# Kernel optimization log

Measured on AMD Instinct MI355X. Metric: run time of the kernel, lower is better.

## Reference

```python
import jax, jax.numpy as jnp
import numpy as np

N, LN, S, T = 50000, 64, 8, 4
E = 800000
MU = 0.9


def setup_inputs() -> dict:
    key = jax.random.key(0)
    ks = jax.random.split(key, 10)
    X_Node = jax.random.randint(ks[0], (E,), 0, N, dtype=jnp.int64) if jax.config.jax_enable_x64 else jax.random.randint(ks[0], (E,), 0, N).astype(jnp.int32)
    X_Neis = jax.random.randint(ks[1], (E,), 0, N).astype(X_Node.dtype)
    dg_list = jax.random.randint(ks[2], (E,), 1, 64).astype(jnp.float32)
    sc = 0.05
    W_emb = jax.random.normal(ks[3], (N, LN), jnp.float32) * sc
    Wxi = jax.random.normal(ks[4], (2 * LN, S * S), jnp.float32) * sc
    bxi = jnp.zeros((S * S,), jnp.float32)
    Wrou = jax.random.normal(ks[5], (LN, S), jnp.float32) * sc
    brou = jnp.zeros((S,), jnp.float32)
    Wout = jax.random.normal(ks[6], (LN + S, 3), jnp.float32) * sc
    bout = jnp.zeros((3,), jnp.float32)
    return {"X_Node": X_Node, "X_Neis": X_Neis, "dg_list": dg_list,
            "W_emb": W_emb, "Wxi": Wxi, "bxi": bxi,
            "Wrou": Wrou, "brou": brou, "Wout": Wout, "bout": bout}


def reference(X_Node, X_Neis, dg_list, W_emb, Wxi, bxi, Wrou, brou, Wout, bout):
    # Edge-wise feature gather: X = [emb[src] || emb[dst]]  -> [E, 2*LN]
    node_e = W_emb[X_Node]
    neis_e = W_emb[X_Neis]
    X = jnp.concatenate([node_e, neis_e], axis=1)
    # Hw precompute (loop-invariant): A [E,S,S], b [E,S]
    A = jnp.tanh(X @ Wxi + bxi).reshape(-1, S, S) * (MU / S) / dg_list[:, None, None]
    b = jnp.tanh(node_e @ Wrou + brou)

    states = jnp.zeros((N, S), dtype=W_emb.dtype)

    def step(states, _):
        H = states[X_Node]                      # gather [E, S]
        H = jnp.einsum('eij,ej->ei', A, H) + b  # per-edge small matvec
        # AggrSum's one-hot [V,E] matmul == scatter-add by X_Node
        new_states = jax.ops.segment_sum(H, X_Node, num_segments=N)
        return new_states, None

    states, _ = jax.lax.scan(step, states, None, length=T)
    logits = jnp.concatenate([W_emb, states], axis=1) @ Wout + bout
    return jax.nn.softmax(logits, axis=1)
```

## Files before the change

### kernel.cpp

```cpp
#include <hip/hip_runtime.h>
#include <hip/hip_fp16.h>
#include <math.h>

#define N_NODES 50000
#define LNDIM   64
#define E_EDGES 800000
#define MU_OVER_S 0.1125f
#define HPAD 16
#define NRANGE 8
#define RANGE_SZ ((N_NODES + NRANGE - 1) / NRANGE)
#define MAXDEG 48
#define BCAP 110000
#define PRE_TPB 256
#define PRE_TILES ((N_NODES + PRE_TPB - 1) / PRE_TPB)
#define LDS_STRIDE 257
#define BK_EPT 16
#define BK_EPB (256 * BK_EPT)
#define BK_NB ((E_EDGES + BK_EPB - 1) / BK_EPB)
#define LOG2E 1.4426950408889634f

typedef _Float16 h2 __attribute__((ext_vector_type(2)));
typedef __fp16   fp16x2 __attribute__((ext_vector_type(2)));

__device__ __forceinline__ h2 bits_h2(unsigned u) {
    union { unsigned x; h2 h; } c; c.x = u; return c.h;
}
__device__ __forceinline__ unsigned h2_bits(h2 h) {
    union { h2 h; unsigned x; } c; c.h = h; return c.x;
}
__device__ __forceinline__ unsigned h2_bits(fp16x2 h) {
    union { fp16x2 h; unsigned x; } c; c.h = h; return c.x;
}

__global__ __launch_bounds__(256) void zero_kernel(int4* __restrict__ p, int n4)
{
    int i = blockIdx.x * 256 + threadIdx.x;
    if (i < n4) p[i] = make_int4(0, 0, 0, 0);
}

__global__ __launch_bounds__(256, 4) void fused_kernel(
    const float* __restrict__ W_emb, const float* __restrict__ Wxi,
    const float* __restrict__ bxi,   const float* __restrict__ Wrou,
    const float* __restrict__ brou,
    const int* __restrict__ X_Node, const int* __restrict__ X_Neis,
    const float* __restrict__ dg_list,
    unsigned short* __restrict__ T1, unsigned short* __restrict__ U,
    float* __restrict__ Bv, int* __restrict__ bkt_cursor,
    uint2* __restrict__ pairs)
{
    __shared__ float ldsT[32 * LDS_STRIDE];
    __shared__ int scnt[4][NRANGE];
    __shared__ int wpref[4][NRANGE];
    __shared__ int gbase[NRANGE];

    int tid = threadIdx.x;

    if (blockIdx.x < BK_NB) {
        int lane = tid & 63;
        int wid  = tid >> 6;
        int wavebase = blockIdx.x * BK_EPB + wid * (BK_EPT * 64);

        unsigned nd[BK_EPT], py[BK_EPT];
        int wcnt[NRANGE];
        #pragma unroll
        for (int r = 0; r < NRANGE; ++r) wcnt[r] = 0;

        #pragma unroll
        for (int i = 0; i < BK_EPT; ++i) {
            int e  = wavebase + i * 64 + lane;
            bool ok = e < E_EDGES;
            int ec = ok ? e : (E_EDGES - 1);
            int node = X_Node[ec];
            unsigned nei = (unsigned)X_Neis[ec];
            float sc = MU_OVER_S / dg_list[ec];
            __half_raw hr = __half_raw(__float2half(sc));
            py[i] = nei | ((unsigned)hr.x << 16);
            int r = ok ? (node / RANGE_SZ) : NRANGE;
            nd[i] = (unsigned)node | ((unsigned)r << 24);
            #pragma unroll
            for (int rr = 0; rr < NRANGE; ++rr)
                wcnt[rr] += __popcll(__ballot(r == rr));
        }

        if (lane < NRANGE) scnt[wid][lane] = wcnt[lane];
        __syncthreads();
        if (tid < NRANGE) {
            int c0 = scnt[0][tid], c1 = scnt[1][tid], c2 = scnt[2][tid], c3 = scnt[3][tid];
            wpref[0][tid] = 0;
            wpref[1][tid] = c0;
            wpref[2][tid] = c0 + c1;
            wpref[3][tid] = c0 + c1 + c2;
            gbase[tid] = atomicAdd(&bkt_cursor[tid * HPAD], c0 + c1 + c2 + c3);
        }
        __syncthreads();

        int wb[NRANGE];
        #pragma unroll
        for (int r = 0; r < NRANGE; ++r) wb[r] = gbase[r] + wpref[wid][r];

        #pragma unroll
        for (int i = 0; i < BK_EPT; ++i) {
            int r = nd[i] >> 24;
            #pragma unroll
            for (int rr = 0; rr < NRANGE; ++rr) {
                unsigned long long m = __ballot(r == rr);
                if (r == rr) {
                    int rank = __popcll(m & ((1ULL << lane) - 1ULL));
                    int pos  = wb[rr] + rank;
                    if (pos < BCAP)
                        pairs[(size_t)rr * BCAP + pos] =
                            make_uint2(nd[i] & 0xFFFFFFu, py[i]);
                }
                wb[rr] += __popcll(m);
            }
        }
        return;
    }

    int pb   = blockIdx.x - BK_NB;
    int pass = pb / PRE_TILES;
    int tile = pb % PRE_TILES;
    int base = tile * PRE_TPB;
    int v    = base + tid;

    if (pass == 4) {
        float acc[8];
        #pragma unroll
        for (int j = 0; j < 8; ++j) acc[j] = brou[j];
        for (int kc = 0; kc < 2; ++kc) {
            __syncthreads();
            #pragma unroll
            for (int c = 0; c < 8; ++c) {
                int idx  = c * PRE_TPB + tid;
                int node = idx >> 3, part = idx & 7;
                int nn   = min(base + node, N_NODES - 1);
                float4 q = *(const float4*)(W_emb + (size_t)nn * 64 + kc * 32 + part * 4);
                ldsT[(part*4+0)*LDS_STRIDE + node] = q.x;
                ldsT[(part*4+1)*LDS_STRIDE + node] = q.y;
                ldsT[(part*4+2)*LDS_STRIDE + node] = q.z;
                ldsT[(part*4+3)*LDS_STRIDE + node] = q.w;
            }
            __syncthreads();
            for (int kk = 0; kk < 32; ++kk) {
                float ek = ldsT[kk * LDS_STRIDE + tid];
                const float* wr = Wrou + (kc*32 + kk) * 8;
                #pragma unroll
                for (int j = 0; j < 8; ++j) acc[j] = fmaf(ek, wr[j], acc[j]);
            }
        }
        if (v < N_NODES) {
            float4* dst = (float4*)(Bv + (size_t)v * 8);
            dst[0] = make_float4(tanhf(acc[0]), tanhf(acc[1]), tanhf(acc[2]), tanhf(acc[3]));
            dst[1] = make_float4(tanhf(acc[4]), tanhf(acc[5]), tanhf(acc[6]), tanhf(acc[7]));
        }
        return;
    }

    int is_u  = pass >> 1;
    int jbase = (pass & 1) * 32;
    const float* W = Wxi + (is_u ? 64 * 64 : 0) + jbase;
    float acc[32];
    if (is_u) {
        #pragma unroll
        for (int j = 0; j < 32; ++j) acc[j] = 0.f;
    } else {
        #pragma unroll
        for (int j = 0; j < 32; ++j) acc[j] = bxi[jbase + j];
    }
    for (int kc = 0; kc < 2; ++kc) {
        __syncthreads();
        #pragma unroll
        for (int c = 0; c < 8; ++c) {
            int idx  = c * PRE_TPB + tid;
            int node = idx >> 3, part = idx & 7;
            int nn   = min(base + node, N_NODES - 1);
            float4 q = *(const float4*)(W_emb + (size_t)nn * 64 + kc * 32 + part * 4);
            ldsT[(part*4+0)*LDS_STRIDE + node] = q.x;
            ldsT[(part*4+1)*LDS_STRIDE + node] = q.y;
            ldsT[(part*4+2)*LDS_STRIDE + node] = q.z;
            ldsT[(part*4+3)*LDS_STRIDE + node] = q.w;
        }
        __syncthreads();
        for (int kk = 0; kk < 32; ++kk) {
            float ek = ldsT[kk * LDS_STRIDE + tid];
            const float* wr = W + (kc*32 + kk) * 64;
            #pragma unroll
            for (int j = 0; j < 32; ++j) acc[j] = fmaf(ek, wr[j], acc[j]);
        }
    }
    if (v >= N_NODES) return;
    unsigned short* outp = is_u ? U : T1;
    uint4* dst = (uint4*)(outp + (size_t)v * 64 + jbase);
    #pragma unroll
    for (int t = 0; t < 4; ++t) {
        uint4 q;
        q.x = h2_bits(__builtin_amdgcn_cvt_pkrtz(acc[8*t+0], acc[8*t+1]));
        q.y = h2_bits(__builtin_amdgcn_cvt_pkrtz(acc[8*t+2], acc[8*t+3]));
        q.z = h2_bits(__builtin_amdgcn_cvt_pkrtz(acc[8*t+4], acc[8*t+5]));
        q.w = h2_bits(__builtin_amdgcn_cvt_pkrtz(acc[8*t+6], acc[8*t+7]));
        dst[t] = q;
    }
}

__global__ __launch_bounds__(256) void scatter2_kernel(
    const uint2* __restrict__ pairs, const int* __restrict__ bkt_cursor,
    int* __restrict__ cnt_arr, unsigned* __restrict__ pk_s)
{
    int r = blockIdx.x & (NRANGE - 1);
    int i = (blockIdx.x >> 3) * 256 + threadIdx.x;
    if (i >= bkt_cursor[r * HPAD]) return;
    uint2 p = pairs[(size_t)r * BCAP + i];
    int pos = atomicAdd(&cnt_arr[(size_t)p.x * HPAD], 1);
    if (pos < MAXDEG) pk_s[(size_t)p.x * MAXDEG + pos] = p.y;
}

__global__ __launch_bounds__(256, 4) void main_kernel(
    const float* __restrict__ W_emb, const float* __restrict__ Wout,
    const float* __restrict__ bout,
    const unsigned short* __restrict__ T1, const unsigned short* __restrict__ U,
    const float* __restrict__ Bv, const int* __restrict__ cnt_arr,
    const unsigned* __restrict__ pk_s, float* __restrict__ out)
{
    int lane = threadIdx.x & 63;
    int wid  = threadIdx.x >> 6;
    int v    = blockIdx.x * 4 + wid;
    if (v >= N_NODES) return;

    int cntv = min(cnt_arr[(size_t)v * HPAD], MAXDEG);
    unsigned pkl = (lane < MAXDEG) ? pk_s[(size_t)v * MAXDEG + lane] : 0u;
    unsigned pk  = (lane < cntv) ? pkl : 0u;
    unsigned tu  = (unsigned)T1[(size_t)v * 64 + lane];
    h2 t2 = bits_h2(tu | (tu << 16));

    const h2 c1 = { (_Float16)0.13333334f,  (_Float16)0.13333334f };
    const h2 c0 = { (_Float16)-0.33333334f, (_Float16)-0.33333334f };

    float m0 = 0.f, m1 = 0.f;

    for (int k0 = 0; k0 < cntv; k0 += 16) {
        unsigned q[16], uu[16];
        #pragma unroll
        for (int x = 0; x < 16; ++x) {
            q[x]  = (unsigned)__builtin_amdgcn_readlane((int)pk, k0 + x);
            uu[x] = (unsigned)U[(size_t)(q[x] & 0xFFFFu) * 64 + lane];
        }
        __builtin_amdgcn_sched_barrier(0);
        #pragma unroll
        for (int p = 0; p < 8; ++p) {
            unsigned sc2 = (q[2*p] >> 16) | (q[2*p+1] & 0xFFFF0000u);
            h2 x   = bits_h2(uu[2*p] | (uu[2*p+1] << 16)) + t2;
            h2 x2  = x * x;
            h2 a   = x2 * c1 + c0;
            h2 th  = (x * x2) * a + x;
            if (p & 1) m1 = __builtin_amdgcn_fdot2(th, bits_h2(sc2), m1, false);
            else       m0 = __builtin_amdgcn_fdot2(th, bits_h2(sc2), m0, false);
        }
    }
    float macc = m0 + m1;

    int   j   = lane & 7;
    int   i   = lane >> 3;
    float cnt = (float)cntv;
    float cj  = cnt * Bv[v * 8 + j];
    float ci  = __shfl(cj, i);
    float sj  = cj;

    #pragma unroll
    for (int step = 0; step < 3; ++step) {
        float p = macc * sj;
        p += __shfl_xor(p, 1);
        p += __shfl_xor(p, 2);
        p += __shfl_xor(p, 4);
        float snew = p + ci;
        sj = __shfl(snew, j * 8);
    }

    float emb = W_emb[(size_t)v * 64 + lane];
    float p0 = emb * Wout[lane * 3 + 0];
    float p1 = emb * Wout[lane * 3 + 1];
    float p2 = emb * Wout[lane * 3 + 2];
    if (lane < 8) {
        p0 = fmaf(sj, Wout[(64 + lane) * 3 + 0], p0);
        p1 = fmaf(sj, Wout[(64 + lane) * 3 + 1], p1);
        p2 = fmaf(sj, Wout[(64 + lane) * 3 + 2], p2);
    }
    #pragma unroll
    for (int m = 1; m < 64; m <<= 1) {
        p0 += __shfl_xor(p0, m);
        p1 += __shfl_xor(p1, m);
        p2 += __shfl_xor(p2, m);
    }
    float L0 = p0 + bout[0], L1 = p1 + bout[1], L2 = p2 + bout[2];
    float mx = fmaxf(L0, fmaxf(L1, L2));
    float e0 = __builtin_amdgcn_exp2f((L0 - mx) * LOG2E);
    float e1 = __builtin_amdgcn_exp2f((L1 - mx) * LOG2E);
    float e2 = __builtin_amdgcn_exp2f((L2 - mx) * LOG2E);
    float inv = __builtin_amdgcn_rcpf(e0 + e1 + e2);
    float rr = (lane == 0) ? e0 : (lane == 1 ? e1 : e2);
    if (lane < 3) out[v * 3 + lane] = rr * inv;
}

extern "C" void kernel_launch(void* const* d_in, const int* in_sizes, int n_in,
                              void* d_out, int out_size, void* d_ws, size_t ws_size,
                              hipStream_t stream)
{
    const int*   X_Node = (const int*)  d_in[0];
    const int*   X_Neis = (const int*)  d_in[1];
    const float* dg     = (const float*)d_in[2];
    const float* W_emb  = (const float*)d_in[3];
    const float* Wxi    = (const float*)d_in[4];
    const float* bxi    = (const float*)d_in[5];
    const float* Wrou   = (const float*)d_in[6];
    const float* brou   = (const float*)d_in[7];
    const float* Wout   = (const float*)d_in[8];
    const float* bout   = (const float*)d_in[9];
    float*       out    = (float*)d_out;

    char*  ws  = (char*)d_ws;
    size_t off = 0;
    auto alloc = [&](size_t bytes) -> void* {
        void* p = ws + off;
        off += (bytes + 255) & ~(size_t)255;
        return p;
    };
    unsigned short* T1       = (unsigned short*)alloc((size_t)N_NODES * 64 * 2);
    unsigned short* U        = (unsigned short*)alloc((size_t)N_NODES * 64 * 2);
    float*          Bv       = (float*)alloc((size_t)N_NODES * 8 * 4);
    int*            cnt_arr  = (int*)  alloc((size_t)N_NODES * HPAD * 4);
    int*            bkt_cur  = (int*)  alloc((size_t)NRANGE * HPAD * 4);
    uint2*          pairs    = (uint2*)alloc((size_t)NRANGE * BCAP * 8);
    unsigned*       pk_s     = (unsigned*)alloc(((size_t)N_NODES * MAXDEG + 64) * 4);

    const int NZ4 = (N_NODES * HPAD + NRANGE * HPAD) / 4;

    zero_kernel<<<(NZ4 + 255) / 256, 256, 0, stream>>>((int4*)cnt_arr, NZ4);
    fused_kernel<<<BK_NB + PRE_TILES * 5, 256, 0, stream>>>(
        W_emb, Wxi, bxi, Wrou, brou, X_Node, X_Neis, dg,
        T1, U, Bv, bkt_cur, pairs);
    scatter2_kernel<<<((BCAP + 255) / 256) * NRANGE, 256, 0, stream>>>(
        pairs, bkt_cur, cnt_arr, pk_s);
    main_kernel<<<(N_NODES + 3) / 4, 256, 0, stream>>>(
        W_emb, Wout, bout, T1, U, Bv, cnt_arr, pk_s, out);
}
```

Baseline: 103.0 us.

## Compute node-level Wxi projections with bf16 MFMA instead of scalar FMAs

Replaces the scalar LDS-transposed fp32 GEMM that built the per-node T1/U projection tables with a wave-level bf16 MFMA (16x16x32) path. Wxi is pre-packed into the MFMA B-operand layout by a prep kernel, which also absorbs the old zeroing kernel. The Wrou/Bv projection becomes its own simple per-thread pass that reads directly from global memory. The aim is to cut the ALU-bound precompute cost and one launch. The trade-off is reduced precision from bf16 inputs and scattered 2-byte output stores.

```diff
diff --git a/kernel.cpp b/kernel.cpp
--- a/kernel.cpp
+++ b/kernel.cpp
@@ -11,44 +11,55 @@
 #define RANGE_SZ ((N_NODES + NRANGE - 1) / NRANGE)
 #define MAXDEG 48
 #define BCAP 110000
-#define PRE_TPB 256
-#define PRE_TILES ((N_NODES + PRE_TPB - 1) / PRE_TPB)
-#define LDS_STRIDE 257
 #define BK_EPT 16
 #define BK_EPB (256 * BK_EPT)
 #define BK_NB ((E_EDGES + BK_EPB - 1) / BK_EPB)
+#define GEMM_NB ((N_NODES + 63) / 64)
+#define BV_TILES ((N_NODES + 255) / 256)
 #define LOG2E 1.4426950408889634f
 
 typedef _Float16 h2 __attribute__((ext_vector_type(2)));
-typedef __fp16   fp16x2 __attribute__((ext_vector_type(2)));
-
+typedef short    bf16x8 __attribute__((ext_vector_type(8)));
+typedef float    f32x4  __attribute__((ext_vector_type(4)));
+
+__device__ __forceinline__ unsigned short f2bf(float f) {
+    unsigned int u = __float_as_uint(f);
+    u = (u + 0x7FFFu + ((u >> 16) & 1u)) >> 16;
+    return (unsigned short)u;
+}
 __device__ __forceinline__ h2 bits_h2(unsigned u) {
     union { unsigned x; h2 h; } c; c.x = u; return c.h;
 }
-__device__ __forceinline__ unsigned h2_bits(h2 h) {
-    union { h2 h; unsigned x; } c; c.h = h; return c.x;
-}
-__device__ __forceinline__ unsigned h2_bits(fp16x2 h) {
-    union { fp16x2 h; unsigned x; } c; c.h = h; return c.x;
-}
-
-__global__ __launch_bounds__(256) void zero_kernel(int4* __restrict__ p, int n4)
-{
-    int i = blockIdx.x * 256 + threadIdx.x;
-    if (i < n4) p[i] = make_int4(0, 0, 0, 0);
+
+__global__ __launch_bounds__(256) void prep_kernel(
+    const float* __restrict__ Wxi, unsigned short* __restrict__ Bpk,
+    int4* __restrict__ zp, int nz4)
+{
+    int gid = blockIdx.x * 256 + threadIdx.x;
+    if (gid < 8192) {
+        int jt = gid >> 10;
+        int rem = gid & 1023;
+        int h = rem >> 9;
+        int rem2 = rem & 511;
+        int l = rem2 >> 3, i = rem2 & 7;
+        int k   = h * 32 + (l >> 4) * 8 + i;
+        int row = (jt >= 4 ? 64 : 0) + k;
+        int col = (jt & 3) * 16 + (l & 15);
+        Bpk[gid] = f2bf(Wxi[row * 64 + col]);
+    }
+    if (gid < nz4) zp[gid] = make_int4(0, 0, 0, 0);
 }
 
 __global__ __launch_bounds__(256, 4) void fused_kernel(
-    const float* __restrict__ W_emb, const float* __restrict__ Wxi,
-    const float* __restrict__ bxi,   const float* __restrict__ Wrou,
-    const float* __restrict__ brou,
+    const float* __restrict__ W_emb, const float* __restrict__ bxi,
+    const float* __restrict__ Wrou,  const float* __restrict__ brou,
     const int* __restrict__ X_Node, const int* __restrict__ X_Neis,
     const float* __restrict__ dg_list,
+    const unsigned short* __restrict__ Bpk,
     unsigned short* __restrict__ T1, unsigned short* __restrict__ U,
-    float* __restrict__ Bv, int* __restrict__ bkt_cursor,
-    uint2* __restrict__ pairs)
-{
-    __shared__ float ldsT[32 * LDS_STRIDE];
+    float* __restrict__ Bv,
+    int* __restrict__ bkt_cursor, uint2* __restrict__ pairs)
+{
     __shared__ int scnt[4][NRANGE];
     __shared__ int wpref[4][NRANGE];
     __shared__ int gbase[NRANGE];
@@ -117,89 +128,82 @@
         return;
     }
 
-    int pb   = blockIdx.x - BK_NB;
-    int pass = pb / PRE_TILES;
-    int tile = pb % PRE_TILES;
-    int base = tile * PRE_TPB;
-    int v    = base + tid;
-
-    if (pass == 4) {
-        float acc[8];
-        #pragma unroll
-        for (int j = 0; j < 8; ++j) acc[j] = brou[j];
-        for (int kc = 0; kc < 2; ++kc) {
-            __syncthreads();
-            #pragma unroll
-            for (int c = 0; c < 8; ++c) {
-                int idx  = c * PRE_TPB + tid;
-                int node = idx >> 3, part = idx & 7;
-                int nn   = min(base + node, N_NODES - 1);
-                float4 q = *(const float4*)(W_emb + (size_t)nn * 64 + kc * 32 + part * 4);
-                ldsT[(part*4+0)*LDS_STRIDE + node] = q.x;
-                ldsT[(part*4+1)*LDS_STRIDE + node] = q.y;
-                ldsT[(part*4+2)*LDS_STRIDE + node] = q.z;
-                ldsT[(part*4+3)*LDS_STRIDE + node] = q.w;
+    if (blockIdx.x < BK_NB + GEMM_NB) {
+        int gb   = blockIdx.x - BK_NB;
+        int lane = tid & 63;
+        int wid  = tid >> 6;
+        int nodebase = gb * 64 + wid * 16;
+        if (nodebase >= N_NODES) return;
+
+        int r0 = lane & 15;
+        int g  = lane >> 4;
+
+        bf16x8 a[2];
+        int arow = min(nodebase + r0, N_NODES - 1);
+        const float* ap = W_emb + (size_t)arow * 64 + g * 8;
+        #pragma unroll
+        for (int h = 0; h < 2; ++h) {
+            float4 q0 = *(const float4*)(ap + h * 32);
+            float4 q1 = *(const float4*)(ap + h * 32 + 4);
+            bf16x8 t;
+            t[0] = (short)f2bf(q0.x); t[1] = (short)f2bf(q0.y);
+            t[2] = (short)f2bf(q0.z); t[3] = (short)f2bf(q0.w);
+            t[4] = (short)f2bf(q1.x); t[5] = (short)f2bf(q1.y);
+            t[6] = (short)f2bf(q1.z); t[7] = (short)f2bf(q1.w);
+            a[h] = t;
+        }
+
+        #pragma unroll
+        for (int jt = 0; jt < 8; ++jt) {
+            float binit = (jt < 4) ? bxi[(jt & 3) * 16 + r0] : 0.f;
+            f32x4 acc;
+            acc[0] = binit; acc[1] = binit; acc[2] = binit; acc[3] = binit;
+            #pragma unroll
+            for (int h = 0; h < 2; ++h) {
+                bf16x8 b = *(const bf16x8*)(Bpk + ((size_t)(jt * 2 + h) * 64 + lane) * 8);
+                acc = __builtin_amdgcn_mfma_f32_16x16x32_bf16(a[h], b, acc, 0, 0, 0);
             }
-            __syncthreads();
-            for (int kk = 0; kk < 32; ++kk) {
-                float ek = ldsT[kk * LDS_STRIDE + tid];
-                const float* wr = Wrou + (kc*32 + kk) * 8;
-                #pragma unroll
-                for (int j = 0; j < 8; ++j) acc[j] = fmaf(ek, wr[j], acc[j]);
+            unsigned short* outp = (jt < 4) ? T1 : U;
+            int jcol = (jt & 3) * 16 + r0;
+            #pragma unroll
+            for (int r = 0; r < 4; ++r) {
+                int node = nodebase + g * 4 + r;
+                if (node < N_NODES) {
+                    union { _Float16 h; unsigned short u; } cv;
+                    cv.h = (_Float16)acc[r];
+                    outp[(size_t)node * 64 + jcol] = cv.u;
+                }
             }
         }
-        if (v < N_NODES) {
-            float4* dst = (float4*)(Bv + (size_t)v * 8);
-            dst[0] = make_float4(tanhf(acc[0]), tanhf(acc[1]), tanhf(acc[2]), tanhf(acc[3]));
-            dst[1] = make_float4(tanhf(acc[4]), tanhf(acc[5]), tanhf(acc[6]), tanhf(acc[7]));
-        }
         return;
     }
 
-    int is_u  = pass >> 1;
-    int jbase = (pass & 1) * 32;
-    const float* W = Wxi + (is_u ? 64 * 64 : 0) + jbase;
-    float acc[32];
-    if (is_u) {
-        #pragma unroll
-        for (int j = 0; j < 32; ++j) acc[j] = 0.f;
-    } else {
-        #pragma unroll
-        for (int j = 0; j < 32; ++j) acc[j] = bxi[jbase + j];
-    }
-    for (int kc = 0; kc < 2; ++kc) {
-        __syncthreads();
-        #pragma unroll
-        for (int c = 0; c < 8; ++c) {
-            int idx  = c * PRE_TPB + tid;
-            int node = idx >> 3, part = idx & 7;
-            int nn   = min(base + node, N_NODES - 1);
-            float4 q = *(const float4*)(W_emb + (size_t)nn * 64 + kc * 32 + part * 4);
-            ldsT[(part*4+0)*LDS_STRIDE + node] = q.x;
-            ldsT[(part*4+1)*LDS_STRIDE + node] = q.y;
-            ldsT[(part*4+2)*LDS_STRIDE + node] = q.z;
-            ldsT[(part*4+3)*LDS_STRIDE + node] = q.w;
-        }
-        __syncthreads();
-        for (int kk = 0; kk < 32; ++kk) {
-            float ek = ldsT[kk * LDS_STRIDE + tid];
-            const float* wr = W + (kc*32 + kk) * 64;
-            #pragma unroll
-            for (int j = 0; j < 32; ++j) acc[j] = fmaf(ek, wr[j], acc[j]);
-        }
-    }
+    int bt = blockIdx.x - (BK_NB + GEMM_NB);
+    int v  = bt * 256 + tid;
     if (v >= N_NODES) return;
-    unsigned short* outp = is_u ? U : T1;
-    uint4* dst = (uint4*)(outp + (size_t)v * 64 + jbase);
+    float acc[8];
     #pragma unroll
-    for (int t = 0; t < 4; ++t) {
-        uint4 q;
-        q.x = h2_bits(__builtin_amdgcn_cvt_pkrtz(acc[8*t+0], acc[8*t+1]));
-        q.y = h2_bits(__builtin_amdgcn_cvt_pkrtz(acc[8*t+2], acc[8*t+3]));
-        q.z = h2_bits(__builtin_amdgcn_cvt_pkrtz(acc[8*t+4], acc[8*t+5]));
-        q.w = h2_bits(__builtin_amdgcn_cvt_pkrtz(acc[8*t+6], acc[8*t+7]));
-        dst[t] = q;
-    }
+    for (int j = 0; j < 8; ++j) acc[j] = brou[j];
+    const float* eb = W_emb + (size_t)v * 64;
+    for (int kc = 0; kc < 4; ++kc) {
+        float e16[16];
+        const float4* er = (const float4*)(eb + kc * 16);
+        #pragma unroll
+        for (int t4 = 0; t4 < 4; ++t4) {
+            float4 q = er[t4];
+            e16[4*t4+0] = q.x; e16[4*t4+1] = q.y; e16[4*t4+2] = q.z; e16[4*t4+3] = q.w;
+        }
+        #pragma unroll
+        for (int kk = 0; kk < 16; ++kk) {
+            float ek = e16[kk];
+            const float* wr = Wrou + (kc * 16 + kk) * 8;
+            #pragma unroll
+            for (int j = 0; j < 8; ++j) acc[j] = fmaf(ek, wr[j], acc[j]);
+        }
+    }
+    float4* dst = (float4*)(Bv + (size_t)v * 8);
+    dst[0] = make_float4(tanhf(acc[0]), tanhf(acc[1]), tanhf(acc[2]), tanhf(acc[3]));
+    dst[1] = make_float4(tanhf(acc[4]), tanhf(acc[5]), tanhf(acc[6]), tanhf(acc[7]));
 }
 
 __global__ __launch_bounds__(256) void scatter2_kernel(
@@ -323,19 +327,20 @@
         off += (bytes + 255) & ~(size_t)255;
         return p;
     };
-    unsigned short* T1       = (unsigned short*)alloc((size_t)N_NODES * 64 * 2);
-    unsigned short* U        = (unsigned short*)alloc((size_t)N_NODES * 64 * 2);
-    float*          Bv       = (float*)alloc((size_t)N_NODES * 8 * 4);
-    int*            cnt_arr  = (int*)  alloc((size_t)N_NODES * HPAD * 4);
-    int*            bkt_cur  = (int*)  alloc((size_t)NRANGE * HPAD * 4);
-    uint2*          pairs    = (uint2*)alloc((size_t)NRANGE * BCAP * 8);
-    unsigned*       pk_s     = (unsigned*)alloc(((size_t)N_NODES * MAXDEG + 64) * 4);
+    unsigned short* T1      = (unsigned short*)alloc((size_t)N_NODES * 64 * 2);
+    unsigned short* U       = (unsigned short*)alloc((size_t)N_NODES * 64 * 2);
+    float*          Bv      = (float*)alloc((size_t)N_NODES * 8 * 4);
+    int*            cnt_arr = (int*)  alloc((size_t)N_NODES * HPAD * 4);
+    int*            bkt_cur = (int*)  alloc((size_t)NRANGE * HPAD * 4);
+    uint2*          pairs   = (uint2*)alloc((size_t)NRANGE * BCAP * 8);
+    unsigned*       pk_s    = (unsigned*)alloc(((size_t)N_NODES * MAXDEG + 64) * 4);
+    unsigned short* Bpk     = (unsigned short*)alloc(8192 * 2);
 
     const int NZ4 = (N_NODES * HPAD + NRANGE * HPAD) / 4;
 
-    zero_kernel<<<(NZ4 + 255) / 256, 256, 0, stream>>>((int4*)cnt_arr, NZ4);
-    fused_kernel<<<BK_NB + PRE_TILES * 5, 256, 0, stream>>>(
-        W_emb, Wxi, bxi, Wrou, brou, X_Node, X_Neis, dg,
+    prep_kernel<<<(NZ4 + 255) / 256, 256, 0, stream>>>(Wxi, Bpk, (int4*)cnt_arr, NZ4);
+    fused_kernel<<<BK_NB + GEMM_NB + BV_TILES, 256, 0, stream>>>(
+        W_emb, bxi, Wrou, brou, X_Node, X_Neis, dg, Bpk,
         T1, U, Bv, bkt_cur, pairs);
     scatter2_kernel<<<((BCAP + 255) / 256) * NRANGE, 256, 0, stream>>>(
         pairs, bkt_cur, cnt_arr, pk_s);
```

Result: faster. 96.50 us (-6.3%).
